# Kernel tuning notes

Hardware: AMD Instinct MI355X
Metric: run time of the kernel (lower is better)

The kernel has to match this reference:

```python
import jax, jax.numpy as jnp
import numpy as np

DECAY = 0.25  # global `decay` in source
EPS = 1e-5    # nn.BatchNorm2d default eps


def quant(x):
    # MultiSpike1: round(clamp(x, 0, 1))
    return jnp.round(jnp.clip(x, 0.0, 1.0))


def lif(x):
    # mem_update: sequential LIF recurrence over time dim T.
    # step0: mem = x[0] (init mem_old=0, spike=0 reproduces it exactly).
    def step(carry, xi):
        mem_old, spike = carry
        mem = (mem_old - jax.lax.stop_gradient(spike) * 0.5) * DECAY + xi
        s = quant(mem)
        return (mem, s), s

    z = jnp.zeros_like(x[0])
    _, out = jax.lax.scan(step, (z, z), x)
    return out  # [T,B,C,H,W]


def setup_inputs() -> dict:
    key = jax.random.key(0)
    k1, k2 = jax.random.split(key, 2)
    T, B, C1, C2, H, W = 4, 8, 64, 128, 128, 128
    x = jax.random.normal(k1, (T, B, C1, H, W), dtype=jnp.float32)
    # Conv2d(c1=64, c2=128, k=3, s=1, pad=1, bias=False)
    conv_w = jax.random.normal(k2, (C2, C1, 3, 3), dtype=jnp.float32) * 0.05
    gamma = jnp.ones((C2,), dtype=jnp.float32)
    beta = jnp.zeros((C2,), dtype=jnp.float32)
    return {"x": x, "conv_w": conv_w, "gamma": gamma, "beta": beta}


def reference(x, conv_w, gamma, beta):
    T, B, C, H, W = x.shape
    C2 = conv_w.shape[0]
    s = lif(x).reshape(T * B, C, H, W)  # flatten(0,1)
    y = jax.lax.conv_general_dilated(
        s, conv_w, window_strides=(1, 1), padding=((1, 1), (1, 1)),
        dimension_numbers=("NCHW", "OIHW", "NCHW"))
    # BatchNorm2d in training mode: batch statistics over (N,H,W), biased var
    mean = y.mean(axis=(0, 2, 3), keepdims=True)
    var = ((y - mean) ** 2).mean(axis=(0, 2, 3), keepdims=True)
    y = (y - mean) * jax.lax.rsqrt(var + EPS)
    y = y * gamma[None, :, None, None] + beta[None, :, None, None]
    return y.reshape(T, B, C2, H, W)
```

## Files before the change

kernel.cpp:

```cpp
#include <hip/hip_runtime.h>

typedef __bf16 bf16x8 __attribute__((ext_vector_type(8)));
typedef float f32x4 __attribute__((ext_vector_type(4)));

#define TBCHW_PLANE 8388608
#define NPIX 524288.0f
#define NBLK 4096
#define SLOT_B 16640

__global__ __launch_bounds__(256) void prep_w(const float* __restrict__ w,
                                              __bf16* __restrict__ wf) {
    int o = blockIdx.x * 256 + threadIdx.x;
    if (o >= 73728) return;
    int j = o & 7;
    int lane = (o >> 3) & 63;
    int mtile = (o >> 9) & 7;
    int kc = o >> 12;
    int k = kc * 32 + (lane >> 4) * 8 + j;
    int c2 = mtile * 16 + (lane & 15);
    int tap = k >> 6, c = k & 63;
    int kh = tap / 3, kw = tap % 3;
    wf[o] = (__bf16)w[((c2 * 64 + c) * 3 + kh) * 3 + kw];
}

__device__ __forceinline__ float lif_step(float& mem, float sp, float xv) {
    mem = (mem - sp * 0.5f) * 0.25f + xv;
    return rintf(fminf(fmaxf(mem, 0.0f), 1.0f));
}

__global__ __launch_bounds__(256) void lif_kernel(const float* __restrict__ x,
                                                  __bf16* __restrict__ s) {
    __shared__ __bf16 lds[2 * 128 * 72];
    int b = blockIdx.x >> 7, h = blockIdx.x & 127;
    int tid = threadIdx.x;

    float4 mem[8], sp[8];
#pragma unroll
    for (int i = 0; i < 8; ++i) { mem[i] = make_float4(0,0,0,0); sp[i] = make_float4(0,0,0,0); }

    for (int half = 0; half < 2; ++half) {
        if (half) __syncthreads();
#pragma unroll
        for (int t2 = 0; t2 < 2; ++t2) {
            int t = half * 2 + t2;
#pragma unroll
            for (int i = 0; i < 8; ++i) {
                int p = tid + 256 * i;
                int c = p >> 5, w0 = (p & 31) * 4;
                const float4 xv = *(const float4*)(x + (size_t)t * TBCHW_PLANE +
                                   (((size_t)b * 64 + c) * 128 + h) * 128 + w0);
                float s0 = lif_step(mem[i].x, sp[i].x, xv.x);
                float s1 = lif_step(mem[i].y, sp[i].y, xv.y);
                float s2 = lif_step(mem[i].z, sp[i].z, xv.z);
                float s3 = lif_step(mem[i].w, sp[i].w, xv.w);
                sp[i] = make_float4(s0, s1, s2, s3);
                __bf16* dst = &lds[(t2 * 128 + w0) * 72 + c];
                dst[0] = (__bf16)s0; dst[72] = (__bf16)s1;
                dst[144] = (__bf16)s2; dst[216] = (__bf16)s3;
            }
        }
        __syncthreads();
#pragma unroll
        for (int i = 0; i < 8; ++i) {
            int u = tid + 256 * i;
            int t2 = u >> 10, inner = u & 1023;
            int w = inner >> 3, c8 = inner & 7;
            bf16x8 v = *(const bf16x8*)&lds[(t2 * 128 + w) * 72 + c8 * 8];
            int n = (half * 2 + t2) * 8 + b;
            *(bf16x8*)(s + (((size_t)n * 128 + h) * 128 + w) * 64 + c8 * 8) = v;
        }
    }
}

__device__ __forceinline__ void stage_row(const __bf16* __restrict__ s, int n, int hh,
                                          char* slot, int tid) {
    if (hh >= 0 && hh < 128) {
        const char* src = (const char*)s + (((size_t)n * 128 + hh) << 14);
#pragma unroll
        for (int i = 0; i < 4; ++i) {
            int g = i * 256 + tid;
            int w = g >> 3;
            int sg = (w << 7) + (((g & 7) ^ ((w + 1) & 7)) << 4);
            __builtin_amdgcn_global_load_lds(
                (const __attribute__((address_space(1))) unsigned int*)(src + sg),
                (__attribute__((address_space(3))) unsigned int*)(slot + 128 + g * 16),
                16, 0, 0);
        }
    } else {
        f32x4 z = {0.f, 0.f, 0.f, 0.f};
#pragma unroll
        for (int i = 0; i < 4; ++i) {
            int g = i * 256 + tid;
            *(f32x4*)(slot + 128 + g * 16) = z;
        }
    }
}

__global__ __launch_bounds__(256, 2) void conv_kernel(const __bf16* __restrict__ s,
                                                      const __bf16* __restrict__ wf,
                                                      float* __restrict__ out,
                                                      float* __restrict__ part) {
    __shared__ __align__(16) char ring[4 * SLOT_B];
    __shared__ float2 P[2][256];
    const int n  = blockIdx.x >> 4;
    const int h0 = (blockIdx.x & 15) << 3;
    const int tid = threadIdx.x;
    const int lane = tid & 63, wave = tid >> 6;
    const int wm = wave >> 1, wn = wave & 1;
    const int lm = lane & 15, q = lane >> 4;

    if (tid < 64) {
        int slot = tid >> 4, col = (tid >> 3) & 1, g8 = tid & 7;
        f32x4 z = {0.f, 0.f, 0.f, 0.f};
        *(f32x4*)(ring + slot * SLOT_B + (col ? 129 * 128 : 0) + g8 * 16) = z;
    }

    bf16x8 ar0[4], ar1[4], ar2[4];
#pragma unroll
    for (int i = 0; i < 4; ++i) {
        ar0[i] = *(const bf16x8*)(wf + (((size_t)0 * 8 + wm * 4 + i) * 64 + lane) * 8);
        ar1[i] = *(const bf16x8*)(wf + (((size_t)1 * 8 + wm * 4 + i) * 64 + lane) * 8);
        ar2[i] = *(const bf16x8*)(wf + (((size_t)2 * 8 + wm * 4 + i) * 64 + lane) * 8);
    }

    stage_row(s, n, h0 - 1, ring + ((h0 + 3) & 3) * SLOT_B, tid);
    stage_row(s, n, h0,     ring + ((h0 + 0) & 3) * SLOT_B, tid);
    stage_row(s, n, h0 + 1, ring + ((h0 + 1) & 3) * SLOT_B, tid);
    __syncthreads();

    const int wbyte = (wn * 64 + lm) * 128;

#pragma unroll 1
    for (int hs = 0; hs < 8; ++hs) {
        const int h = h0 + hs;
        if (hs < 7) stage_row(s, n, h + 2, ring + ((h + 2) & 3) * SLOT_B, tid);

        const char* rb0 = ring + ((h + 3) & 3) * SLOT_B;
        const char* rb1 = ring + ((h + 0) & 3) * SLOT_B;
        const char* rb2 = ring + ((h + 1) & 3) * SLOT_B;

        f32x4 acc[4][4];
#pragma unroll
        for (int i = 0; i < 4; ++i)
#pragma unroll
            for (int j = 0; j < 4; ++j)
#pragma unroll
                for (int e = 0; e < 4; ++e) acc[i][j][e] = 0.0f;

#pragma unroll
        for (int kc = 0; kc < 18; ++kc) {
            const int tap = kc >> 1;
            const int kh = tap / 3, kw = tap - kh * 3;
            const int c8b = (kc & 1) * 4;
            const char* rb = (kh == 0) ? rb0 : (kh == 1) ? rb1 : rb2;
            const int off = kw * 128 + ((((c8b + q) ^ ((lm + kw) & 7))) << 4);
            bf16x8 av[4], bv[4];
#pragma unroll
            for (int i = 0; i < 4; ++i)
                av[i] = (kc == 0) ? ar0[i] : (kc == 1) ? ar1[i] : (kc == 2) ? ar2[i]
                      : *(const bf16x8*)(wf + (((size_t)kc * 8 + wm * 4 + i) * 64 + lane) * 8);
#pragma unroll
            for (int j = 0; j < 4; ++j)
                bv[j] = *(const bf16x8*)(rb + wbyte + j * 2048 + off);
#pragma unroll
            for (int i = 0; i < 4; ++i)
#pragma unroll
                for (int j = 0; j < 4; ++j)
                    acc[i][j] = __builtin_amdgcn_mfma_f32_16x16x32_bf16(av[i], bv[j], acc[i][j], 0, 0, 0);
        }

#pragma unroll
        for (int i = 0; i < 4; ++i) {
#pragma unroll
            for (int r = 0; r < 4; ++r) {
                int c2 = wm * 64 + i * 16 + q * 4 + r;
                size_t ob = ((size_t)(n * 128 + c2) * 128 + h) * 128 + wn * 64 + lm;
                float sum = 0.0f, ssq = 0.0f;
#pragma unroll
                for (int j = 0; j < 4; ++j) {
                    float v = acc[i][j][r];
                    out[ob + j * 16] = v;
                    sum += v; ssq += v * v;
                }
#pragma unroll
                for (int d = 8; d > 0; d >>= 1) {
                    sum += __shfl_down(sum, d);
                    ssq += __shfl_down(ssq, d);
                }
                if (lm == 0)
                    P[hs & 1][wave * 64 + i * 16 + q * 4 + r] = make_float2(sum, ssq);
            }
        }
        __syncthreads();
        {
            int stat = tid >> 7, c2x = tid & 127;
            int wp = c2x >> 6, idx = c2x & 63;
            float2 a2 = P[hs & 1][(wp * 2) * 64 + idx];
            float2 b2 = P[hs & 1][(wp * 2 + 1) * 64 + idx];
            float val = stat ? (a2.y + b2.y) : (a2.x + b2.x);
            part[(size_t)tid * NBLK + (blockIdx.x << 3) + hs] = val;
        }
    }
}

__global__ __launch_bounds__(256) void reduce_stats(const float* __restrict__ part,
                                                    const float* __restrict__ gamma,
                                                    const float* __restrict__ beta,
                                                    float* __restrict__ ss) {
    int c = blockIdx.x;
    int tid = threadIdx.x;
    const float* ps = part + (size_t)c * NBLK;
    const float* pq = part + (size_t)(128 + c) * NBLK;
    float sum = 0.0f, ssq = 0.0f;
    for (int i = tid; i < NBLK; i += 256) { sum += ps[i]; ssq += pq[i]; }
#pragma unroll
    for (int d = 32; d > 0; d >>= 1) {
        sum += __shfl_down(sum, d);
        ssq += __shfl_down(ssq, d);
    }
    __shared__ float2 wred[4];
    if ((tid & 63) == 0) wred[tid >> 6] = make_float2(sum, ssq);
    __syncthreads();
    if (tid == 0) {
        float S = 0.0f, Q = 0.0f;
#pragma unroll
        for (int w2 = 0; w2 < 4; ++w2) { S += wred[w2].x; Q += wred[w2].y; }
        const float inv = 1.0f / NPIX;
        float mean = S * inv;
        float var = Q * inv - mean * mean;
        float sc = gamma[c] * rsqrtf(var + 1e-5f);
        ss[c] = sc;
        ss[128 + c] = beta[c] - mean * sc;
    }
}

__global__ __launch_bounds__(256) void bn_apply(float* __restrict__ out,
                                                const float* __restrict__ ss) {
    size_t i4 = (size_t)blockIdx.x * 256 + threadIdx.x;
    int c2 = (int)((i4 >> 12) & 127);
    float sc = ss[c2], sh = ss[128 + c2];
    float4* p = (float4*)out + i4;
    float4 v = *p;
    v.x = v.x * sc + sh; v.y = v.y * sc + sh;
    v.z = v.z * sc + sh; v.w = v.w * sc + sh;
    *p = v;
}

extern "C" void kernel_launch(void* const* d_in, const int* in_sizes, int n_in,
                              void* d_out, int out_size, void* d_ws, size_t ws_size,
                              hipStream_t stream) {
    const float* x     = (const float*)d_in[0];
    const float* cw    = (const float*)d_in[1];
    const float* gamma = (const float*)d_in[2];
    const float* beta  = (const float*)d_in[3];
    float* out = (float*)d_out;

    char* ws = (char*)d_ws;
    __bf16* s     = (__bf16*)ws;
    __bf16* wfrag = (__bf16*)(ws + 67108864);
    float*  part  = (float*)(ws + 67108864 + 147456);
    float*  ss    = part + 256 * NBLK;

    prep_w      <<<288,   256, 0, stream>>>(cw, wfrag);
    lif_kernel  <<<1024,  256, 0, stream>>>(x, s);
    conv_kernel <<<512,   256, 0, stream>>>(s, wfrag, out, part);
    reduce_stats<<<128,   256, 0, stream>>>(part, gamma, beta, ss);
    bn_apply    <<<65536, 256, 0, stream>>>(out, ss);
}
```

Measured before the change: 641.1 us.

## Compute one output row per conv block and use grid-stride BN apply

The conv kernel now runs 4096 blocks, each computing a single output row. Each block stages its three input rows into LDS at once instead of looping over eight rows with a 4-slot ring buffer, and block IDs are swizzled across XCDs. Occupancy rises to 3 blocks per CU. The cost is that each input row is loaded three times instead of roughly once, and there is no load/compute overlap within a block. Separately, bn_apply becomes a 2048-block grid-stride loop instead of 65536 blocks.

```diff
diff --git a/kernel.cpp b/kernel.cpp
--- a/kernel.cpp
+++ b/kernel.cpp
@@ -72,134 +72,115 @@
     }
 }
 
-__device__ __forceinline__ void stage_row(const __bf16* __restrict__ s, int n, int hh,
-                                          char* slot, int tid) {
-    if (hh >= 0 && hh < 128) {
-        const char* src = (const char*)s + (((size_t)n * 128 + hh) << 14);
-#pragma unroll
-        for (int i = 0; i < 4; ++i) {
-            int g = i * 256 + tid;
-            int w = g >> 3;
-            int sg = (w << 7) + (((g & 7) ^ ((w + 1) & 7)) << 4);
-            __builtin_amdgcn_global_load_lds(
-                (const __attribute__((address_space(1))) unsigned int*)(src + sg),
-                (__attribute__((address_space(3))) unsigned int*)(slot + 128 + g * 16),
-                16, 0, 0);
-        }
-    } else {
-        f32x4 z = {0.f, 0.f, 0.f, 0.f};
-#pragma unroll
-        for (int i = 0; i < 4; ++i) {
-            int g = i * 256 + tid;
-            *(f32x4*)(slot + 128 + g * 16) = z;
-        }
-    }
-}
-
-__global__ __launch_bounds__(256, 2) void conv_kernel(const __bf16* __restrict__ s,
+__global__ __launch_bounds__(256, 3) void conv_kernel(const __bf16* __restrict__ s,
                                                       const __bf16* __restrict__ wf,
                                                       float* __restrict__ out,
                                                       float* __restrict__ part) {
-    __shared__ __align__(16) char ring[4 * SLOT_B];
-    __shared__ float2 P[2][256];
-    const int n  = blockIdx.x >> 4;
-    const int h0 = (blockIdx.x & 15) << 3;
+    __shared__ __align__(16) char sb3[3 * SLOT_B];
+    const int p = blockIdx.x;
+    const int bid = (p & 7) * 512 + (p >> 3);
+    const int n = bid >> 7, h = bid & 127;
     const int tid = threadIdx.x;
+
+#pragma unroll
+    for (int r = 0; r < 3; ++r) {
+        int hh = h + r - 1;
+        char* slot = sb3 + r * SLOT_B;
+        if (hh >= 0 && hh < 128) {
+            const char* src = (const char*)s + (((size_t)n * 128 + hh) << 14);
+#pragma unroll
+            for (int i = 0; i < 4; ++i) {
+                int g = i * 256 + tid;
+                int w = g >> 3;
+                int sg = (w << 7) + (((g & 7) ^ ((w + 1) & 7)) << 4);
+                __builtin_amdgcn_global_load_lds(
+                    (const __attribute__((address_space(1))) unsigned int*)(src + sg),
+                    (__attribute__((address_space(3))) unsigned int*)(slot + 128 + g * 16),
+                    16, 0, 0);
+            }
+        } else {
+            f32x4 z = {0.f, 0.f, 0.f, 0.f};
+#pragma unroll
+            for (int i = 0; i < 4; ++i)
+                *(f32x4*)(slot + 128 + (i * 256 + tid) * 16) = z;
+        }
+    }
+    if (tid < 48) {
+        int r = tid / 16, q16 = tid % 16;
+        int col = q16 & 1, g8 = q16 >> 1;
+        f32x4 z = {0.f, 0.f, 0.f, 0.f};
+        *(f32x4*)(sb3 + r * SLOT_B + (col ? 129 * 128 : 0) + g8 * 16) = z;
+    }
+    __syncthreads();
+
     const int lane = tid & 63, wave = tid >> 6;
     const int wm = wave >> 1, wn = wave & 1;
     const int lm = lane & 15, q = lane >> 4;
-
-    if (tid < 64) {
-        int slot = tid >> 4, col = (tid >> 3) & 1, g8 = tid & 7;
-        f32x4 z = {0.f, 0.f, 0.f, 0.f};
-        *(f32x4*)(ring + slot * SLOT_B + (col ? 129 * 128 : 0) + g8 * 16) = z;
-    }
-
-    bf16x8 ar0[4], ar1[4], ar2[4];
+    const int wbyte = (wn * 64 + lm) * 128;
+
+    f32x4 acc[4][4];
+#pragma unroll
+    for (int i = 0; i < 4; ++i)
+#pragma unroll
+        for (int j = 0; j < 4; ++j)
+#pragma unroll
+            for (int e = 0; e < 4; ++e) acc[i][j][e] = 0.0f;
+
+#pragma unroll
+    for (int kc = 0; kc < 18; ++kc) {
+        const int tap = kc >> 1;
+        const int kh = tap / 3, kw = tap - kh * 3;
+        const int c8b = (kc & 1) * 4;
+        const char* rb = sb3 + kh * SLOT_B;
+        const int off = kw * 128 + (((c8b + q) ^ ((lm + kw) & 7)) << 4);
+        bf16x8 a[4], bb[4];
+#pragma unroll
+        for (int i = 0; i < 4; ++i)
+            a[i] = *(const bf16x8*)(wf + (((size_t)kc * 8 + wm * 4 + i) * 64 + lane) * 8);
+#pragma unroll
+        for (int j = 0; j < 4; ++j)
+            bb[j] = *(const bf16x8*)(rb + wbyte + j * 2048 + off);
+#pragma unroll
+        for (int i = 0; i < 4; ++i)
+#pragma unroll
+            for (int j = 0; j < 4; ++j)
+                acc[i][j] = __builtin_amdgcn_mfma_f32_16x16x32_bf16(a[i], bb[j], acc[i][j], 0, 0, 0);
+    }
+
+    __syncthreads();
+    float2* P = (float2*)sb3;
+
 #pragma unroll
     for (int i = 0; i < 4; ++i) {
-        ar0[i] = *(const bf16x8*)(wf + (((size_t)0 * 8 + wm * 4 + i) * 64 + lane) * 8);
-        ar1[i] = *(const bf16x8*)(wf + (((size_t)1 * 8 + wm * 4 + i) * 64 + lane) * 8);
-        ar2[i] = *(const bf16x8*)(wf + (((size_t)2 * 8 + wm * 4 + i) * 64 + lane) * 8);
-    }
-
-    stage_row(s, n, h0 - 1, ring + ((h0 + 3) & 3) * SLOT_B, tid);
-    stage_row(s, n, h0,     ring + ((h0 + 0) & 3) * SLOT_B, tid);
-    stage_row(s, n, h0 + 1, ring + ((h0 + 1) & 3) * SLOT_B, tid);
-    __syncthreads();
-
-    const int wbyte = (wn * 64 + lm) * 128;
-
-#pragma unroll 1
-    for (int hs = 0; hs < 8; ++hs) {
-        const int h = h0 + hs;
-        if (hs < 7) stage_row(s, n, h + 2, ring + ((h + 2) & 3) * SLOT_B, tid);
-
-        const char* rb0 = ring + ((h + 3) & 3) * SLOT_B;
-        const char* rb1 = ring + ((h + 0) & 3) * SLOT_B;
-        const char* rb2 = ring + ((h + 1) & 3) * SLOT_B;
-
-        f32x4 acc[4][4];
-#pragma unroll
-        for (int i = 0; i < 4; ++i)
-#pragma unroll
-            for (int j = 0; j < 4; ++j)
-#pragma unroll
-                for (int e = 0; e < 4; ++e) acc[i][j][e] = 0.0f;
-
-#pragma unroll
-        for (int kc = 0; kc < 18; ++kc) {
-            const int tap = kc >> 1;
-            const int kh = tap / 3, kw = tap - kh * 3;
-            const int c8b = (kc & 1) * 4;
-            const char* rb = (kh == 0) ? rb0 : (kh == 1) ? rb1 : rb2;
-            const int off = kw * 128 + ((((c8b + q) ^ ((lm + kw) & 7))) << 4);
-            bf16x8 av[4], bv[4];
-#pragma unroll
-            for (int i = 0; i < 4; ++i)
-                av[i] = (kc == 0) ? ar0[i] : (kc == 1) ? ar1[i] : (kc == 2) ? ar2[i]
-                      : *(const bf16x8*)(wf + (((size_t)kc * 8 + wm * 4 + i) * 64 + lane) * 8);
-#pragma unroll
-            for (int j = 0; j < 4; ++j)
-                bv[j] = *(const bf16x8*)(rb + wbyte + j * 2048 + off);
-#pragma unroll
-            for (int i = 0; i < 4; ++i)
-#pragma unroll
-                for (int j = 0; j < 4; ++j)
-                    acc[i][j] = __builtin_amdgcn_mfma_f32_16x16x32_bf16(av[i], bv[j], acc[i][j], 0, 0, 0);
-        }
-
-#pragma unroll
-        for (int i = 0; i < 4; ++i) {
-#pragma unroll
-            for (int r = 0; r < 4; ++r) {
-                int c2 = wm * 64 + i * 16 + q * 4 + r;
-                size_t ob = ((size_t)(n * 128 + c2) * 128 + h) * 128 + wn * 64 + lm;
-                float sum = 0.0f, ssq = 0.0f;
-#pragma unroll
-                for (int j = 0; j < 4; ++j) {
-                    float v = acc[i][j][r];
-                    out[ob + j * 16] = v;
-                    sum += v; ssq += v * v;
-                }
-#pragma unroll
-                for (int d = 8; d > 0; d >>= 1) {
-                    sum += __shfl_down(sum, d);
-                    ssq += __shfl_down(ssq, d);
-                }
-                if (lm == 0)
-                    P[hs & 1][wave * 64 + i * 16 + q * 4 + r] = make_float2(sum, ssq);
-            }
-        }
-        __syncthreads();
-        {
-            int stat = tid >> 7, c2x = tid & 127;
-            int wp = c2x >> 6, idx = c2x & 63;
-            float2 a2 = P[hs & 1][(wp * 2) * 64 + idx];
-            float2 b2 = P[hs & 1][(wp * 2 + 1) * 64 + idx];
-            float val = stat ? (a2.y + b2.y) : (a2.x + b2.x);
-            part[(size_t)tid * NBLK + (blockIdx.x << 3) + hs] = val;
-        }
+#pragma unroll
+        for (int r = 0; r < 4; ++r) {
+            int c2 = wm * 64 + i * 16 + q * 4 + r;
+            size_t ob = ((size_t)(n * 128 + c2) * 128 + h) * 128 + wn * 64 + lm;
+            float sum = 0.0f, ssq = 0.0f;
+#pragma unroll
+            for (int j = 0; j < 4; ++j) {
+                float v = acc[i][j][r];
+                out[ob + j * 16] = v;
+                sum += v; ssq += v * v;
+            }
+#pragma unroll
+            for (int d = 8; d > 0; d >>= 1) {
+                sum += __shfl_down(sum, d);
+                ssq += __shfl_down(ssq, d);
+            }
+            if (lm == 0) {
+                P[wave * 64 + i * 16 + q * 4 + r] = make_float2(sum, ssq);
+            }
+        }
+    }
+    __syncthreads();
+    {
+        int stat = tid >> 7, c2x = tid & 127;
+        int wp = c2x >> 6, idx = c2x & 63;
+        float2 a2 = P[(wp * 2) * 64 + idx];
+        float2 b2 = P[(wp * 2 + 1) * 64 + idx];
+        float val = stat ? (a2.y + b2.y) : (a2.x + b2.x);
+        part[(size_t)tid * NBLK + bid] = val;
     }
 }
 
@@ -236,14 +217,16 @@
 
 __global__ __launch_bounds__(256) void bn_apply(float* __restrict__ out,
                                                 const float* __restrict__ ss) {
-    size_t i4 = (size_t)blockIdx.x * 256 + threadIdx.x;
-    int c2 = (int)((i4 >> 12) & 127);
-    float sc = ss[c2], sh = ss[128 + c2];
-    float4* p = (float4*)out + i4;
-    float4 v = *p;
-    v.x = v.x * sc + sh; v.y = v.y * sc + sh;
-    v.z = v.z * sc + sh; v.w = v.w * sc + sh;
-    *p = v;
+    const size_t stride = (size_t)2048 * 256;
+    for (size_t i4 = (size_t)blockIdx.x * 256 + threadIdx.x; i4 < 16777216; i4 += stride) {
+        int c2 = (int)((i4 >> 12) & 127);
+        float sc = ss[c2], sh = ss[128 + c2];
+        float4* p = (float4*)out + i4;
+        float4 v = *p;
+        v.x = v.x * sc + sh; v.y = v.y * sc + sh;
+        v.z = v.z * sc + sh; v.w = v.w * sc + sh;
+        *p = v;
+    }
 }
 
 extern "C" void kernel_launch(void* const* d_in, const int* in_sizes, int n_in,
@@ -263,7 +246,7 @@
 
     prep_w      <<<288,   256, 0, stream>>>(cw, wfrag);
     lif_kernel  <<<1024,  256, 0, stream>>>(x, s);
-    conv_kernel <<<512,   256, 0, stream>>>(s, wfrag, out, part);
+    conv_kernel <<<NBLK,  256, 0, stream>>>(s, wfrag, out, part);
     reduce_stats<<<128,   256, 0, stream>>>(part, gamma, beta, ss);
-    bn_apply    <<<65536, 256, 0, stream>>>(out, ss);
-}
+    bn_apply    <<<2048,  256, 0, stream>>>(out, ss);
+}
```

Result: faster. 541.3 us (-15.6%).
